# Performance work log

Hardware: AMD Instinct MI355X
Metric: run time of the kernel (lower is better)

## Reference

```python
import jax, jax.numpy as jnp
import numpy as np

D = 1024; NH = 16; HD = 64; FF = 4096; DEPTH = 4
P = 14; C = 3; GRID = 32; MERGE = 2; NIMG = 4
L = GRID * GRID; S = NIMG * L; ORIG = 24; EPS = 1e-6
SCALE = HD ** -0.5


def setup_inputs() -> dict:
    key = jax.random.key(0)
    ks = jax.random.split(key, 12)
    s = 0.02
    return {
        "pixel_values": jax.random.normal(ks[0], (S, C * P * P), jnp.float32),
        "grid_thw": jnp.tile(jnp.array([[1, GRID, GRID]], jnp.int32), (NIMG, 1)),
        "conv_w": jax.random.normal(ks[1], (D, C * P * P), jnp.float32) * s,
        "conv_b": jnp.zeros((D,), jnp.float32),
        "pos_embed": jax.random.normal(ks[2], (ORIG * ORIG, D), jnp.float32) * s,
        "ln1_g": jnp.ones((DEPTH, D), jnp.float32),
        "ln1_b": jnp.zeros((DEPTH, D), jnp.float32),
        "qkv_w": jax.random.normal(ks[3], (DEPTH, 3 * D, D), jnp.float32) * s,
        "qkv_b": jnp.zeros((DEPTH, 3 * D), jnp.float32),
        "proj_w": jax.random.normal(ks[4], (DEPTH, D, D), jnp.float32) * s,
        "proj_b": jnp.zeros((DEPTH, D), jnp.float32),
        "ln2_g": jnp.ones((DEPTH, D), jnp.float32),
        "ln2_b": jnp.zeros((DEPTH, D), jnp.float32),
        "fc1_w": jax.random.normal(ks[5], (DEPTH, FF, D), jnp.float32) * s,
        "fc1_b": jnp.zeros((DEPTH, FF), jnp.float32),
        "fc2_w": jax.random.normal(ks[6], (DEPTH, D, FF), jnp.float32) * s,
        "fc2_b": jnp.zeros((DEPTH, D), jnp.float32),
    }


def _pos_ids():
    # rot_pos_emb spatial-merge permutation for one t=1 image, tiled over images
    h = jnp.broadcast_to(jnp.arange(GRID)[:, None], (GRID, GRID))
    w = jnp.broadcast_to(jnp.arange(GRID)[None, :], (GRID, GRID))
    def perm(a):
        a = a.reshape(GRID // MERGE, MERGE, GRID // MERGE, MERGE)
        return a.transpose(0, 2, 1, 3).reshape(-1)
    hpos = jnp.tile(perm(h), NIMG)  # [S]
    wpos = jnp.tile(perm(w), NIMG)
    return hpos, wpos


def _bilinear_border(img, nx, ny):
    # img [H, W, D]; nx, ny in [-1, 1]; align_corners=False, padding_mode='border'
    Hh, Ww, _ = img.shape
    x = (nx + 1.0) * 0.5 * Ww - 0.5
    y = (ny + 1.0) * 0.5 * Hh - 0.5
    x0 = jnp.floor(x); y0 = jnp.floor(y)
    wx = (x - x0)[:, None]; wy = (y - y0)[:, None]
    x0i = jnp.clip(x0.astype(jnp.int32), 0, Ww - 1)
    x1i = jnp.clip(x0.astype(jnp.int32) + 1, 0, Ww - 1)
    y0i = jnp.clip(y0.astype(jnp.int32), 0, Hh - 1)
    y1i = jnp.clip(y0.astype(jnp.int32) + 1, 0, Hh - 1)
    v00 = img[y0i, x0i]; v01 = img[y0i, x1i]
    v10 = img[y1i, x0i]; v11 = img[y1i, x1i]
    return (v00 * (1 - wy) * (1 - wx) + v01 * (1 - wy) * wx
            + v10 * wy * (1 - wx) + v11 * wy * wx)


def _ln(x, g, b):
    m = jnp.mean(x, axis=-1, keepdims=True)
    v = jnp.mean(jnp.square(x - m), axis=-1, keepdims=True)
    return (x - m) * jax.lax.rsqrt(v + EPS) * g + b


def _forward(pixel_values, conv_w, conv_b, pos_embed, ln1_g, ln1_b, qkv_w, qkv_b,
             proj_w, proj_b, ln2_g, ln2_b, fc1_w, fc1_b, fc2_w, fc2_b):
    # patch embed: conv with kernel==stride==patch over one patch == linear
    x = pixel_values @ conv_w.T + conv_b  # [S, D]

    # interpolated 2D position embedding (grid_sample bilinear, border pad)
    hpos, wpos = _pos_ids()
    norm_w = (wpos.astype(jnp.float32) + 0.5) / GRID * 2.0 - 1.0
    norm_h = (hpos.astype(jnp.float32) + 0.5) / GRID * 2.0 - 1.0
    pe = _bilinear_border(pos_embed.reshape(ORIG, ORIG, D), norm_w, norm_h)
    x = x + pe

    for i in range(DEPTH):
        # attention (block-diagonal over equal-length images -> batched)
        r = x
        y = _ln(x, ln1_g[i], ln1_b[i])
        qkv = (y @ qkv_w[i].T + qkv_b[i]).reshape(NIMG, L, 3, NH, HD)
        q = qkv[:, :, 0].transpose(0, 2, 1, 3)  # [B, H, L, hd]
        k = qkv[:, :, 1].transpose(0, 2, 1, 3)
        v = qkv[:, :, 2].transpose(0, 2, 1, 3)
        scores = jnp.einsum('bhqd,bhkd->bhqk', q, k) * SCALE
        probs = jax.nn.softmax(scores, axis=-1)
        o = jnp.einsum('bhqk,bhkd->bhqd', probs, v)
        o = o.transpose(0, 2, 1, 3).reshape(S, D)
        x = r + o @ proj_w[i].T + proj_b[i]
        # MLP
        r = x
        y = _ln(x, ln2_g[i], ln2_b[i])
        h = jax.nn.gelu(y @ fc1_w[i].T + fc1_b[i], approximate=False)
        x = r + h @ fc2_w[i].T + fc2_b[i]
    return x


def reference(pixel_values, grid_thw, conv_w, conv_b, pos_embed, ln1_g, ln1_b,
              qkv_w, qkv_b, proj_w, proj_b, ln2_g, ln2_b, fc1_w, fc1_b, fc2_w, fc2_b):
    return _forward(pixel_values, conv_w, conv_b, pos_embed, ln1_g, ln1_b, qkv_w,
                    qkv_b, proj_w, proj_b, ln2_g, ln2_b, fc1_w, fc1_b, fc2_w, fc2_b)
```

## Files before the change

### kernel.cpp

```cpp
#include <hip/hip_runtime.h>
#include <math.h>

typedef __bf16 bf16x8 __attribute__((ext_vector_type(8)));
typedef float f32x4 __attribute__((ext_vector_type(4)));
typedef short s16x4 __attribute__((ext_vector_type(4)));
typedef short s16x8 __attribute__((ext_vector_type(8)));

static __device__ __forceinline__ short f2bs(float f) {
  return __builtin_bit_cast(short, (__bf16)f);
}

#define GLL16(gp, lp) __builtin_amdgcn_global_load_lds( \
    (const __attribute__((address_space(1))) void*)(gp), \
    (__attribute__((address_space(3))) void*)(lp), 16, 0, 0)

__global__ __launch_bounds__(256) void cvt_f32_bf16(const float* __restrict__ s,
                                                    short* __restrict__ d, int n) {
  int stride = gridDim.x * blockDim.x * 4;
  for (int j = (blockIdx.x * blockDim.x + threadIdx.x) * 4; j < n; j += stride) {
    float4 v = *(const float4*)(s + j);
    s16x4 o;
    o[0] = f2bs(v.x); o[1] = f2bs(v.y); o[2] = f2bs(v.z); o[3] = f2bs(v.w);
    *(s16x4*)(d + j) = o;
  }
}

__global__ __launch_bounds__(256) void cvt_pad(const float* __restrict__ s,
                                               short* __restrict__ d) {
  int r = blockIdx.x;
  for (int c = threadIdx.x; c < 608; c += blockDim.x)
    d[(size_t)r * 608 + c] = (c < 588) ? f2bs(s[(size_t)r * 588 + c]) : (short)0;
}

template <int N, int K, int EPI, int CM, int CN>
__global__ __launch_bounds__(256) void gemm_bt(const short* __restrict__ A,
                                               const short* __restrict__ B,
                                               const float* __restrict__ bias,
                                               const float* __restrict__ resid,
                                               void* __restrict__ out) {
  static_assert(K % 32 == 0, "K");
  constexpr int NT = K / 32;
  static_assert(NT >= 3, "pipeline depth");
  constexpr int NX = N / 128, NY = 32;
  constexpr int nwg = NX * NY;
  static_assert(nwg % 8 == 0 && (nwg / 8) % (CM * CN) == 0, "chunk");
  static_assert(NX % CN == 0 && NY % CM == 0, "cells");
  __shared__ short lA[3][128 * 32];
  __shared__ short lB[3][128 * 32];

  const int o = blockIdx.x;
  const int wid = (o & 7) * (nwg / 8) + (o >> 3);
  constexpr int cellsz = CM * CN;
  const int cell = wid / cellsz, within = wid % cellsz;
  constexpr int cellsx = NX / CN;
  const int bm0 = ((cell / cellsx) * CM + within / CN) * 128;
  const int bn0 = ((cell % cellsx) * CN + within % CN) * 128;

  const int t = threadIdx.x, w = t >> 6, lane = t & 63;
  const int wr = w >> 1, wc = w & 1;
  f32x4 acc[4][4] = {};

  const int srow = t >> 2;
  const int scol = ((t & 3) ^ ((srow >> 1) & 3)) * 8;
  const short* aP = A + (size_t)(bm0 + srow) * K + scol;
  const short* bP = B + (size_t)(bn0 + srow) * K + scol;
  const int sdst0 = (w * 16) * 32;
  const int sdst1 = (64 + w * 16) * 32;

  const int lr = lane & 15;
  const int qx = ((lane >> 4) ^ ((lr >> 1) & 3)) * 8;

  auto stage = [&](int buf, int ko) {
    GLL16(aP + ko, &lA[buf][sdst0]);
    GLL16(aP + ko + (size_t)64 * K, &lA[buf][sdst1]);
    GLL16(bP + ko, &lB[buf][sdst0]);
    GLL16(bP + ko + (size_t)64 * K, &lB[buf][sdst1]);
  };

  stage(0, 0);
  stage(1, 32);
  stage(2, 64);

  int buf = 0;
  for (int kt = 0; kt < NT; ++kt) {
    if (kt < NT - 2)       asm volatile("s_waitcnt vmcnt(8)" ::: "memory");
    else if (kt == NT - 2) asm volatile("s_waitcnt vmcnt(4)" ::: "memory");
    else                   asm volatile("s_waitcnt vmcnt(0)" ::: "memory");
    __builtin_amdgcn_s_barrier();
    asm volatile("" ::: "memory");
    __builtin_amdgcn_sched_barrier(0);

    bf16x8 af[4], bg[4];
#pragma unroll
    for (int mi = 0; mi < 4; ++mi)
      af[mi] = *(const bf16x8*)&lA[buf][(wr * 64 + mi * 16 + lr) * 32 + qx];
#pragma unroll
    for (int ni = 0; ni < 4; ++ni)
      bg[ni] = *(const bf16x8*)&lB[buf][(wc * 64 + ni * 16 + lr) * 32 + qx];

    asm volatile("s_waitcnt lgkmcnt(0)" ::: "memory");
    __builtin_amdgcn_sched_barrier(0);
    __builtin_amdgcn_s_barrier();
    asm volatile("" ::: "memory");
    __builtin_amdgcn_sched_barrier(0);

    if (kt + 3 < NT) stage(buf, (kt + 3) * 32);
    __builtin_amdgcn_sched_barrier(0);

#pragma unroll
    for (int mi = 0; mi < 4; ++mi)
#pragma unroll
      for (int ni = 0; ni < 4; ++ni)
        acc[mi][ni] = __builtin_amdgcn_mfma_f32_16x16x32_bf16(af[mi], bg[ni],
                                                              acc[mi][ni], 0, 0, 0);
    buf = (buf == 2) ? 0 : buf + 1;
  }

  const int lg4 = (lane >> 4) * 4;
#pragma unroll
  for (int mi = 0; mi < 4; ++mi) {
#pragma unroll
    for (int ni = 0; ni < 4; ++ni) {
      const int row = bm0 + wr * 64 + mi * 16 + lg4;
      const int col = bn0 + wc * 64 + ni * 16 + lr;
      const float bc = bias[col];
#pragma unroll
      for (int r = 0; r < 4; ++r) {
        float v = acc[mi][ni][r] + bc;
        size_t idx = (size_t)(row + r) * N + col;
        if constexpr (EPI == 1) v = 0.5f * v * (1.0f + erff(v * 0.70710678118f));
        if constexpr (EPI == 0 || EPI == 1) ((short*)out)[idx] = f2bs(v);
        else if constexpr (EPI == 2) ((float*)out)[idx] = v + resid[idx];
        else ((float*)out)[idx] = v;
      }
    }
  }
}

template <int N, int KC, int LDK, int EPI, int CM, int CN, int KSPLIT>
__global__ __launch_bounds__(512, 2) void gemm256(const short* __restrict__ A,
                                                  const short* __restrict__ B,
                                                  const float* __restrict__ bias,
                                                  void* __restrict__ out) {
  static_assert(KC % 64 == 0, "K");
  constexpr int NKT = KC / 64;
  static_assert(NKT >= 2, "ktiles");
  constexpr int NXT = N / 256, MYT = 16;
  constexpr int nwg = NXT * MYT * KSPLIT;
  constexpr int cellsz = CM * CN;
  static_assert(nwg % 8 == 0 && (nwg / 8) % cellsz == 0, "chunk");
  static_assert((NXT * MYT) % cellsz == 0, "cellspace");
  static_assert(NXT % CN == 0 && MYT % CM == 0, "cells");

  __shared__ short sA[2][2][8192];
  __shared__ short sB[2][2][8192];

  const int o = blockIdx.x;
  const int wid = (o & 7) * (nwg / 8) + (o >> 3);
  const int kc = wid / (NXT * MYT);
  const int rem = wid % (NXT * MYT);
  const int cell = rem / cellsz, within = rem % cellsz;
  constexpr int cellsx = NXT / CN;
  const int bm0 = ((cell / cellsx) * CM + within / CN) * 256;
  const int bn0 = ((cell % cellsx) * CN + within % CN) * 256;

  const int tid = threadIdx.x, wv = tid >> 6, lane = tid & 63;
  const int wrow = wv >> 2, wcol = wv & 3;
  const int lr = lane & 15, lg = lane >> 4;

  const int sr0 = tid >> 2;
  const int sc0 = ((tid & 3) ^ ((sr0 >> 1) & 3)) * 8;
  const short* aS0 = A + (size_t)(bm0 + sr0) * LDK + kc * KC + sc0;
  const short* bS0 = B + (size_t)(bn0 + sr0) * LDK + kc * KC + sc0;
  const int ld0 = wv * 512, ld1 = 4096 + wv * 512;

  auto stageA = [&](int d, int h, int kt) {
    const int off = kt * 64 + h * 32;
    GLL16(aS0 + off, &sA[d][h][ld0]);
    GLL16(aS0 + off + (size_t)128 * LDK, &sA[d][h][ld1]);
  };
  auto stageB = [&](int d, int h, int kt) {
    const int off = kt * 64 + h * 32;
    GLL16(bS0 + off, &sB[d][h][ld0]);
    GLL16(bS0 + off + (size_t)128 * LDK, &sB[d][h][ld1]);
  };

  const int chR = (lg ^ ((lr >> 1) & 3)) * 8;
  const int rA0 = wrow * 128 + lr;
  const int rB0 = wcol * 64 + lr;

  f32x4 acc[8][4] = {};
  bf16x8 aF[4][2], bF[4][2];

  stageA(0, 0, 0); stageA(0, 1, 0);
  stageB(0, 0, 0); stageB(0, 1, 0);
  asm volatile("s_waitcnt vmcnt(0)" ::: "memory");
  __builtin_amdgcn_s_barrier();

#define RD_A(mh)                                                              \
  _Pragma("unroll")                                                           \
  for (int f = 0; f < 4; ++f) {                                               \
    aF[f][0] = *(const bf16x8*)&sA[r][0][(rA0 + (mh)*64 + f * 16) * 32 + chR];\
    aF[f][1] = *(const bf16x8*)&sA[r][1][(rA0 + (mh)*64 + f * 16) * 32 + chR];\
  }
#define RD_B2(n0)                                                             \
  _Pragma("unroll")                                                           \
  for (int n = 0; n < 2; ++n) {                                               \
    bF[(n0)+n][0] = *(const bf16x8*)&sB[r][0][(rB0 + ((n0)+n) * 16) * 32 + chR];\
    bF[(n0)+n][1] = *(const bf16x8*)&sB[r][1][(rB0 + ((n0)+n) * 16) * 32 + chR];\
  }
#define MM(ab, n0)                                                            \
  __builtin_amdgcn_s_setprio(1);                                              \
  _Pragma("unroll")                                                           \
  for (int ks = 0; ks < 2; ++ks)                                              \
    _Pragma("unroll")                                                         \
    for (int f = 0; f < 4; ++f)                                               \
      _Pragma("unroll")                                                       \
      for (int n = 0; n < 2; ++n)                                             \
        acc[(ab)+f][(n0)+n] = __builtin_amdgcn_mfma_f32_16x16x32_bf16(        \
            aF[f][ks], bF[(n0)+n][ks], acc[(ab)+f][(n0)+n], 0, 0, 0);         \
  __builtin_amdgcn_s_setprio(0);
#define BAR __builtin_amdgcn_s_barrier();
#define LGW asm volatile("s_waitcnt lgkmcnt(0)");

  for (int t = 0; t < NKT; ++t) {
    const int r = t & 1, sd = r ^ 1;
    const bool more = (t + 1 < NKT);
    RD_A(0); RD_B2(0);
    if (more) { stageA(sd, 0, t + 1); stageA(sd, 1, t + 1); }
    BAR; LGW; MM(0, 0); BAR;
    RD_B2(2);
    if (more) { stageB(sd, 0, t + 1); stageB(sd, 1, t + 1); }
    BAR; LGW; MM(0, 2); BAR;
    RD_A(1);
    BAR; LGW; MM(4, 2); BAR;
    MM(4, 0);
    asm volatile("s_waitcnt vmcnt(0)" ::: "memory");
    BAR;
  }
#undef RD_A
#undef RD_B2
#undef MM
#undef BAR
#undef LGW

  const int lg4 = lg * 4;
#pragma unroll
  for (int mh = 0; mh < 2; ++mh) {
#pragma unroll
    for (int f = 0; f < 4; ++f) {
#pragma unroll
      for (int n = 0; n < 4; ++n) {
        const int row = bm0 + wrow * 128 + mh * 64 + f * 16 + lg4;
        const int col = bn0 + wcol * 64 + n * 16 + lr;
        float bc = 0.f;
        if constexpr (EPI != 5) bc = bias[col];
#pragma unroll
        for (int r = 0; r < 4; ++r) {
          float v = acc[mh * 4 + f][n][r] + bc;
          if constexpr (EPI == 1) {
            const float u = v * (0.7978845608f + 0.0356774081f * v * v);
            v = v / (1.0f + __expf(-2.0f * u));
          }
          if constexpr (EPI == 5)
            ((float*)out)[((size_t)kc << 22) + (size_t)(row + r) * N + col] = v;
          else
            ((short*)out)[(size_t)(row + r) * N + col] = f2bs(v);
        }
      }
    }
  }
}

__global__ __launch_bounds__(256) void fc2_reduce(const float* __restrict__ part,
                                                  const float* __restrict__ bias,
                                                  const float* __restrict__ resid,
                                                  float* __restrict__ dest) {
  const size_t i4 = ((size_t)blockIdx.x * 256 + threadIdx.x) * 4;
  const float4 a0 = *(const float4*)(part + i4);
  const float4 a1 = *(const float4*)(part + (1ull << 22) + i4);
  const float4 a2 = *(const float4*)(part + (2ull << 22) + i4);
  const float4 a3 = *(const float4*)(part + (3ull << 22) + i4);
  const float4 rv = *(const float4*)(resid + i4);
  const float4 bv = *(const float4*)(bias + (i4 & 1023));
  float4 o;
  o.x = a0.x + a1.x + a2.x + a3.x + rv.x + bv.x;
  o.y = a0.y + a1.y + a2.y + a3.y + rv.y + bv.y;
  o.z = a0.z + a1.z + a2.z + a3.z + rv.z + bv.z;
  o.w = a0.w + a1.w + a2.w + a3.w + rv.w + bv.w;
  *(float4*)(dest + i4) = o;
}

__global__ __launch_bounds__(256) void ln_fwd(const float* __restrict__ x,
                                              const float* __restrict__ g,
                                              const float* __restrict__ b,
                                              short* __restrict__ y) {
  const int row = blockIdx.x, t = threadIdx.x, w = t >> 6, lane = t & 63;
  const float4 v = ((const float4*)(x + (size_t)row * 1024))[t];
  float s = v.x + v.y + v.z + v.w;
  float ss = v.x * v.x + v.y * v.y + v.z * v.z + v.w * v.w;
#pragma unroll
  for (int m = 1; m < 64; m <<= 1) { s += __shfl_xor(s, m); ss += __shfl_xor(ss, m); }
  __shared__ float rs[4], rss[4];
  if (lane == 0) { rs[w] = s; rss[w] = ss; }
  __syncthreads();
  s = rs[0] + rs[1] + rs[2] + rs[3];
  ss = rss[0] + rss[1] + rss[2] + rss[3];
  const float mean = s * (1.f / 1024.f);
  const float var = ss * (1.f / 1024.f) - mean * mean;
  const float rstd = rsqrtf(var + 1e-6f);
  const float4 gv = ((const float4*)g)[t];
  const float4 bv = ((const float4*)b)[t];
  s16x4 o;
  o[0] = f2bs((v.x - mean) * rstd * gv.x + bv.x);
  o[1] = f2bs((v.y - mean) * rstd * gv.y + bv.y);
  o[2] = f2bs((v.z - mean) * rstd * gv.z + bv.z);
  o[3] = f2bs((v.w - mean) * rstd * gv.w + bv.w);
  *(s16x4*)(y + (size_t)row * 1024 + t * 4) = o;
}

__global__ __launch_bounds__(256) void pos_add(float* __restrict__ x,
                                               const float* __restrict__ pe) {
  const int sidx = blockIdx.x;
  const int f = sidx & 1023;
  const int wq = 2 * ((f >> 2) & 15) + (f & 1);
  const int hq = 2 * (f >> 6) + ((f >> 1) & 1);
  const float gx = (wq + 0.5f) * 0.75f - 0.5f;
  const float gy = (hq + 0.5f) * 0.75f - 0.5f;
  const float fx = floorf(gx), fy = floorf(gy);
  const float wx = gx - fx, wy = gy - fy;
  int x0 = (int)fx, y0 = (int)fy;
  const int x0i = x0 < 0 ? 0 : (x0 > 23 ? 23 : x0);
  const int x1i = (x0 + 1) < 0 ? 0 : ((x0 + 1) > 23 ? 23 : x0 + 1);
  const int y0i = y0 < 0 ? 0 : (y0 > 23 ? 23 : y0);
  const int y1i = (y0 + 1) < 0 ? 0 : ((y0 + 1) > 23 ? 23 : y0 + 1);
  const float w00 = (1 - wy) * (1 - wx), w01 = (1 - wy) * wx;
  const float w10 = wy * (1 - wx), w11 = wy * wx;
  const int c = threadIdx.x * 4;
  const float4 p00 = *(const float4*)(pe + (size_t)(y0i * 24 + x0i) * 1024 + c);
  const float4 p01 = *(const float4*)(pe + (size_t)(y0i * 24 + x1i) * 1024 + c);
  const float4 p10 = *(const float4*)(pe + (size_t)(y1i * 24 + x0i) * 1024 + c);
  const float4 p11 = *(const float4*)(pe + (size_t)(y1i * 24 + x1i) * 1024 + c);
  float* xp = x + (size_t)sidx * 1024 + c;
  float4 xv = *(float4*)xp;
  xv.x += w00 * p00.x + w01 * p01.x + w10 * p10.x + w11 * p11.x;
  xv.y += w00 * p00.y + w01 * p01.y + w10 * p10.y + w11 * p11.y;
  xv.z += w00 * p00.z + w01 * p01.z + w10 * p10.z + w11 * p11.z;
  xv.w += w00 * p00.w + w01 * p01.w + w10 * p10.w + w11 * p11.w;
  *(float4*)xp = xv;
}

__global__ __launch_bounds__(256) void attn_fwd(const short* __restrict__ qkv,
                                                short* __restrict__ outp) {
  __shared__ short lK[2][64 * 64];
  __shared__ short Vt[2][64 * 72];
  const int t = threadIdx.x, w = t >> 6, lane = t & 63;
  const int b = blockIdx.y >> 4, h = blockIdx.y & 15;
  const int sbase = b * 1024;
  const int q0 = blockIdx.x * 64 + w * 16;
  const int lr = lane & 15, lg = lane >> 4;

  const short* qrow = qkv + (size_t)(sbase + q0 + lr) * 3072 + h * 64;
  const bf16x8 qf0 = *(const bf16x8*)(qrow + lg * 8);
  const bf16x8 qf1 = *(const bf16x8*)(qrow + 32 + lg * 8);

  const int krofs = t >> 3;
  const int kcol = ((t & 7) ^ (krofs & 7)) * 8;
  const short* ksrc = qkv + (size_t)(sbase + krofs) * 3072 + 1024 + h * 64 + kcol;
  const int vkv = t >> 2, vdp = t & 3;
  const short* vsrc = qkv + (size_t)(sbase + vkv) * 3072 + 2048 + h * 64 + vdp * 16;
  const int vph = vkv ^ (vdp << 4);

  f32x4 o[4] = {};
  float mrun = -1e30f, lsum = 0.f;

  s16x8 v0 = *(const s16x8*)vsrc;
  s16x8 v1 = *(const s16x8*)(vsrc + 8);
  GLL16(ksrc, &lK[0][(w * 8) * 64]);
  GLL16(ksrc + (size_t)32 * 3072, &lK[0][(32 + w * 8) * 64]);
#pragma unroll
  for (int j = 0; j < 8; ++j) Vt[0][(vdp * 16 + j) * 72 + vph] = v0[j];
#pragma unroll
  for (int j = 0; j < 8; ++j) Vt[0][(vdp * 16 + 8 + j) * 72 + vph] = v1[j];
  asm volatile("s_waitcnt vmcnt(0) lgkmcnt(0)" ::: "memory");
  __builtin_amdgcn_s_barrier();

  int buf = 0;
  for (int kb = 0; kb < 16; ++kb) {
    if (kb < 15) {
      const short* vs = vsrc + (size_t)(kb + 1) * 64 * 3072;
      v0 = *(const s16x8*)vs;
      v1 = *(const s16x8*)(vs + 8);
      const short* ks = ksrc + (size_t)(kb + 1) * 64 * 3072;
      GLL16(ks, &lK[buf ^ 1][(w * 8) * 64]);
      GLL16(ks + (size_t)32 * 3072, &lK[buf ^ 1][(32 + w * 8) * 64]);
    }

    f32x4 s[4];
    __builtin_amdgcn_s_setprio(1);
#pragma unroll
    for (int sub = 0; sub < 4; ++sub) {
      const int krow = (sub * 16 + lr) * 64;
      const bf16x8 kf0 = *(const bf16x8*)&lK[buf][krow + (lg ^ (lr & 7)) * 8];
      const bf16x8 kf1 = *(const bf16x8*)&lK[buf][krow + ((lg + 4) ^ (lr & 7)) * 8];
      f32x4 a = {};
      a = __builtin_amdgcn_mfma_f32_16x16x32_bf16(kf0, qf0, a, 0, 0, 0);
      a = __builtin_amdgcn_mfma_f32_16x16x32_bf16(kf1, qf1, a, 0, 0, 0);
      s[sub] = a;
    }
    __builtin_amdgcn_s_setprio(0);

    constexpr float SC = 0.125f * 1.44269504089f;
    float sl[16];
#pragma unroll
    for (int sub = 0; sub < 4; ++sub)
#pragma unroll
      for (int r = 0; r < 4; ++r) sl[sub * 4 + r] = s[sub][r] * SC;
    float tm = sl[0];
#pragma unroll
    for (int i = 1; i < 16; ++i) tm = fmaxf(tm, sl[i]);
    tm = fmaxf(tm, __shfl_xor(tm, 16));
    tm = fmaxf(tm, __shfl_xor(tm, 32));
    if (!__all(tm <= mrun + 12.0f)) {
      const float newm = fmaxf(mrun, tm);
      const float sc = exp2f(mrun - newm);
      lsum *= sc;
#pragma unroll
      for (int f = 0; f < 4; ++f) {
        o[f][0] *= sc; o[f][1] *= sc; o[f][2] *= sc; o[f][3] *= sc;
      }
      mrun = newm;
    }
    s16x4 pb[4];
    float psum = 0.f;
#pragma unroll
    for (int sub = 0; sub < 4; ++sub)
#pragma unroll
      for (int r = 0; r < 4; ++r) {
        const float p = exp2f(sl[sub * 4 + r] - mrun);
        psum += p;
        pb[sub][r] = f2bs(p);
      }
    psum += __shfl_xor(psum, 16);
    psum += __shfl_xor(psum, 32);
    lsum += psum;

    __builtin_amdgcn_s_setprio(1);
#pragma unroll
    for (int f = 0; f < 4; ++f) {
      const int vrow = (f * 16 + lr) * 72;
#pragma unroll
      for (int sub = 0; sub < 4; ++sub) {
        const s16x4 va = *(const s16x4*)&Vt[buf][vrow + ((sub ^ f) << 4) + lg * 4];
        o[f] = __builtin_amdgcn_mfma_f32_16x16x16bf16_1k(va, pb[sub], o[f], 0, 0, 0);
      }
    }
    __builtin_amdgcn_s_setprio(0);

    if (kb < 15) {
#pragma unroll
      for (int j = 0; j < 8; ++j) Vt[buf ^ 1][(vdp * 16 + j) * 72 + vph] = v0[j];
#pragma unroll
      for (int j = 0; j < 8; ++j) Vt[buf ^ 1][(vdp * 16 + 8 + j) * 72 + vph] = v1[j];
      asm volatile("s_waitcnt vmcnt(0) lgkmcnt(0)" ::: "memory");
      __builtin_amdgcn_s_barrier();
      buf ^= 1;
    }
  }

  const float inv = 1.0f / lsum;
  short* orow = outp + (size_t)(sbase + q0 + lr) * 1024 + h * 64;
#pragma unroll
  for (int f = 0; f < 4; ++f) {
    s16x4 ov;
    ov[0] = f2bs(o[f][0] * inv); ov[1] = f2bs(o[f][1] * inv);
    ov[2] = f2bs(o[f][2] * inv); ov[3] = f2bs(o[f][3] * inv);
    *(s16x4*)(orow + f * 16 + lg * 4) = ov;
  }
}

extern "C" void kernel_launch(void* const* d_in, const int* in_sizes, int n_in,
                              void* d_out, int out_size, void* d_ws, size_t ws_size,
                              hipStream_t stream) {
  const float* pixel  = (const float*)d_in[0];
  const float* conv_w = (const float*)d_in[2];
  const float* conv_b = (const float*)d_in[3];
  const float* pos_e  = (const float*)d_in[4];
  const float* ln1_g  = (const float*)d_in[5];
  const float* ln1_b  = (const float*)d_in[6];
  const float* qkv_w  = (const float*)d_in[7];
  const float* qkv_b  = (const float*)d_in[8];
  const float* proj_w = (const float*)d_in[9];
  const float* proj_b = (const float*)d_in[10];
  const float* ln2_g  = (const float*)d_in[11];
  const float* ln2_b  = (const float*)d_in[12];
  const float* fc1_w  = (const float*)d_in[13];
  const float* fc1_b  = (const float*)d_in[14];
  const float* fc2_w  = (const float*)d_in[15];
  const float* fc2_b  = (const float*)d_in[16];

  char* ws = (char*)d_ws;
  short* wQKV  = (short*)(ws + 0);
  short* wPROJ = (short*)(ws + 25165824);
  short* wFC1  = (short*)(ws + 33554432);
  short* wFC2  = (short*)(ws + 67108864);
  float* X     = (float*)(ws + 100663296);
  short* Y     = (short*)(ws + 117440512);
  short* QKVB  = (short*)(ws + 125829120);
  short* ATTNO = (short*)(ws + 150994944);
  short* H     = QKVB;
  short* WPIX  = QKVB;
  short* WCONV = (short*)(ws + 125829120 + 4980736);
  float* PART  = (float*)(ws + 159383552);
  const bool wsbig = ws_size >= (size_t)159383552 + 67108864;

  cvt_f32_bf16<<<2048, 256, 0, stream>>>(qkv_w, wQKV, 4 * 3072 * 1024);
  cvt_f32_bf16<<<1024, 256, 0, stream>>>(proj_w, wPROJ, 4 * 1024 * 1024);
  cvt_f32_bf16<<<2048, 256, 0, stream>>>(fc1_w, wFC1, 4 * 4096 * 1024);
  cvt_f32_bf16<<<2048, 256, 0, stream>>>(fc2_w, wFC2, 4 * 1024 * 4096);
  cvt_pad<<<4096, 256, 0, stream>>>(pixel, WPIX);
  cvt_pad<<<1024, 256, 0, stream>>>(conv_w, WCONV);

  gemm_bt<1024, 608, 3, 4, 8><<<256, 256, 0, stream>>>(WPIX, WCONV, conv_b, nullptr, X);
  pos_add<<<4096, 256, 0, stream>>>(X, pos_e);

  for (int i = 0; i < 4; ++i) {
    ln_fwd<<<4096, 256, 0, stream>>>(X, ln1_g + i * 1024, ln1_b + i * 1024, Y);
    gemm256<3072, 1024, 1024, 0, 8, 3, 1><<<192, 512, 0, stream>>>(
        Y, wQKV + (size_t)i * 3072 * 1024, qkv_b + i * 3072, QKVB);
    attn_fwd<<<dim3(16, 64), 256, 0, stream>>>(QKVB, ATTNO);
    gemm_bt<1024, 1024, 2, 4, 8><<<256, 256, 0, stream>>>(
        ATTNO, wPROJ + (size_t)i * 1024 * 1024, proj_b + i * 1024, X, X);
    ln_fwd<<<4096, 256, 0, stream>>>(X, ln2_g + i * 1024, ln2_b + i * 1024, Y);
    gemm256<4096, 1024, 1024, 1, 8, 4, 1><<<256, 512, 0, stream>>>(
        Y, wFC1 + (size_t)i * 4096 * 1024, fc1_b + i * 4096, H);
    float* dest = (i < 3) ? X : (float*)d_out;
    if (wsbig) {
      gemm256<1024, 1024, 4096, 5, 8, 4, 4><<<256, 512, 0, stream>>>(
          H, wFC2 + (size_t)i * 1024 * 4096, nullptr, PART);
      fc2_reduce<<<4096, 256, 0, stream>>>(PART, fc2_b + i * 1024, X, dest);
    } else {
      gemm_bt<1024, 4096, 2, 4, 8><<<256, 256, 0, stream>>>(
          H, wFC2 + (size_t)i * 1024 * 4096, fc2_b + i * 1024, X, dest);
    }
  }
}
```

Baseline: 973.6 us.

## Split-K proj GEMM with new 128-tile kernel and fuse residual reduce into LayerNorm

Adds a 128x128-tile split-K GEMM kernel for the attention output projection, which writes four fp32 partials. A new reduce_ln kernel sums those partials with bias and residual, writes X, and computes the next LayerNorm in the same pass. The same fusion is applied after the fc2 split-K reduce, so the standalone ln_fwd launches and their extra read of X go away. The cost is more partial-buffer traffic for proj (4x fp32 writes) in exchange for better occupancy with 1024 workgroups.

Result: no change. 990.0 us (+1.7%).

```diff
diff --git a/kernel.cpp b/kernel.cpp
--- a/kernel.cpp
+++ b/kernel.cpp
@@ -132,6 +132,120 @@
         if constexpr (EPI == 0 || EPI == 1) ((short*)out)[idx] = f2bs(v);
         else if constexpr (EPI == 2) ((float*)out)[idx] = v + resid[idx];
         else ((float*)out)[idx] = v;
+      }
+    }
+  }
+}
+
+template <int N, int KC, int LDK, int EPI, int CM, int CN, int KSPLIT>
+__global__ __launch_bounds__(256, 2) void gemm128(const short* __restrict__ A,
+                                                  const short* __restrict__ B,
+                                                  const float* __restrict__ bias,
+                                                  void* __restrict__ out) {
+  static_assert(KC % 64 == 0, "K");
+  constexpr int NKT = KC / 64;
+  static_assert(NKT >= 4 && (NKT % 2) == 0, "ktiles");
+  constexpr int NX = N / 128, NY = 32;
+  constexpr int nwg = NX * NY * KSPLIT;
+  constexpr int cellsz = CM * CN;
+  static_assert(nwg % 8 == 0 && (nwg / 8) % cellsz == 0, "chunk");
+  static_assert((NX * NY) % cellsz == 0, "cellspace");
+  static_assert(NX % CN == 0 && NY % CM == 0, "cells");
+
+  __shared__ short sA[2][128 * 64];
+  __shared__ short sB[2][128 * 64];
+
+  const int o = blockIdx.x;
+  const int wid = (o & 7) * (nwg / 8) + (o >> 3);
+  const int kc = wid / (NX * NY);
+  const int rem = wid % (NX * NY);
+  const int cell = rem / cellsz, within = rem % cellsz;
+  constexpr int cellsx = NX / CN;
+  const int bm0 = ((cell / cellsx) * CM + within / CN) * 128;
+  const int bn0 = ((cell % cellsx) * CN + within % CN) * 128;
+
+  const int t = threadIdx.x, w = t >> 6, lane = t & 63;
+  const int wr = w >> 1, wc = w & 1;
+  const int lr = lane & 15, lg = lane >> 4;
+
+  const int srow = t >> 3;
+  const int sch = (t & 7) ^ (srow & 7);
+  const short* aS = A + (size_t)(bm0 + srow) * LDK + kc * KC + sch * 8;
+  const short* bS = B + (size_t)(bn0 + srow) * LDK + kc * KC + sch * 8;
+  const int ldst = w * 512;
+
+  auto stage = [&](int d, int kt) {
+    const size_t ko = (size_t)kt * 64;
+#pragma unroll
+    for (int q = 0; q < 4; ++q)
+      GLL16(aS + (size_t)q * 32 * LDK + ko, &sA[d][q * 2048 + ldst]);
+#pragma unroll
+    for (int q = 0; q < 4; ++q)
+      GLL16(bS + (size_t)q * 32 * LDK + ko, &sB[d][q * 2048 + ldst]);
+  };
+
+  f32x4 acc[4][4] = {};
+
+  stage(0, 0);
+  stage(1, 1);
+
+#define TILE(tt, dd)                                                          \
+  {                                                                           \
+    if ((tt) + 1 < NKT) asm volatile("s_waitcnt vmcnt(8)" ::: "memory");      \
+    else                asm volatile("s_waitcnt vmcnt(0)" ::: "memory");      \
+    __builtin_amdgcn_s_barrier();                                             \
+    bf16x8 af[2][4], bf[2][4];                                                \
+    _Pragma("unroll")                                                         \
+    for (int ks = 0; ks < 2; ++ks) {                                          \
+      _Pragma("unroll")                                                       \
+      for (int mi = 0; mi < 4; ++mi)                                          \
+        af[ks][mi] = *(const bf16x8*)&sA[dd][(wr * 64 + mi * 16 + lr) * 64 +  \
+                                             (((ks << 2) + lg) ^ (lr & 7)) * 8]; \
+      _Pragma("unroll")                                                       \
+      for (int ni = 0; ni < 4; ++ni)                                          \
+        bf[ks][ni] = *(const bf16x8*)&sB[dd][(wc * 64 + ni * 16 + lr) * 64 +  \
+                                             (((ks << 2) + lg) ^ (lr & 7)) * 8]; \
+    }                                                                         \
+    __builtin_amdgcn_s_setprio(1);                                            \
+    _Pragma("unroll")                                                         \
+    for (int ks = 0; ks < 2; ++ks)                                            \
+      _Pragma("unroll")                                                       \
+      for (int mi = 0; mi < 4; ++mi)                                          \
+        _Pragma("unroll")                                                     \
+        for (int ni = 0; ni < 4; ++ni)                                        \
+          acc[mi][ni] = __builtin_amdgcn_mfma_f32_16x16x32_bf16(              \
+              af[ks][mi], bf[ks][ni], acc[mi][ni], 0, 0, 0);                  \
+    __builtin_amdgcn_s_setprio(0);                                            \
+    __builtin_amdgcn_s_barrier();                                             \
+    if ((tt) + 2 < NKT) stage(dd, (tt) + 2);                                  \
+  }
+
+  for (int kt = 0; kt < NKT; kt += 2) {
+    TILE(kt, 0);
+    TILE(kt + 1, 1);
+  }
+#undef TILE
+
+  const int lg4 = lg * 4;
+#pragma unroll
+  for (int mi = 0; mi < 4; ++mi) {
+#pragma unroll
+    for (int ni = 0; ni < 4; ++ni) {
+      const int row = bm0 + wr * 64 + mi * 16 + lg4;
+      const int col = bn0 + wc * 64 + ni * 16 + lr;
+      float bc = 0.f;
+      if constexpr (EPI != 5) bc = bias[col];
+#pragma unroll
+      for (int r = 0; r < 4; ++r) {
+        float v = acc[mi][ni][r] + bc;
+        if constexpr (EPI == 1) {
+          const float u = v * (0.7978845608f + 0.0356774081f * v * v);
+          v = v / (1.0f + __expf(-2.0f * u));
+        }
+        if constexpr (EPI == 5)
+          ((float*)out)[((size_t)kc << 22) + (size_t)(row + r) * N + col] = v;
+        else
+          ((short*)out)[(size_t)(row + r) * N + col] = f2bs(v);
       }
     }
   }
@@ -289,6 +403,50 @@
   o.z = a0.z + a1.z + a2.z + a3.z + rv.z + bv.z;
   o.w = a0.w + a1.w + a2.w + a3.w + rv.w + bv.w;
   *(float4*)(dest + i4) = o;
+}
+
+__global__ __launch_bounds__(256) void reduce_ln(const float* __restrict__ part,
+                                                 const float* __restrict__ bias,
+                                                 const float* __restrict__ resid,
+                                                 const float* __restrict__ g,
+                                                 const float* __restrict__ b,
+                                                 float* __restrict__ X,
+                                                 short* __restrict__ Y) {
+  const int row = blockIdx.x, t = threadIdx.x, w = t >> 6, lane = t & 63;
+  const size_t i4 = (size_t)row * 1024 + t * 4;
+  const float4 a0 = *(const float4*)(part + i4);
+  const float4 a1 = *(const float4*)(part + (1ull << 22) + i4);
+  const float4 a2 = *(const float4*)(part + (2ull << 22) + i4);
+  const float4 a3 = *(const float4*)(part + (3ull << 22) + i4);
+  const float4 rv = *(const float4*)(resid + i4);
+  const float4 bv = *(const float4*)(bias + t * 4);
+  float4 v;
+  v.x = a0.x + a1.x + a2.x + a3.x + rv.x + bv.x;
+  v.y = a0.y + a1.y + a2.y + a3.y + rv.y + bv.y;
+  v.z = a0.z + a1.z + a2.z + a3.z + rv.z + bv.z;
+  v.w = a0.w + a1.w + a2.w + a3.w + rv.w + bv.w;
+  *(float4*)(X + i4) = v;
+
+  float s = v.x + v.y + v.z + v.w;
+  float ss = v.x * v.x + v.y * v.y + v.z * v.z + v.w * v.w;
+#pragma unroll
+  for (int m = 1; m < 64; m <<= 1) { s += __shfl_xor(s, m); ss += __shfl_xor(ss, m); }
+  __shared__ float rs[4], rss[4];
+  if (lane == 0) { rs[w] = s; rss[w] = ss; }
+  __syncthreads();
+  s = rs[0] + rs[1] + rs[2] + rs[3];
+  ss = rss[0] + rss[1] + rss[2] + rss[3];
+  const float mean = s * (1.f / 1024.f);
+  const float var = ss * (1.f / 1024.f) - mean * mean;
+  const float rstd = rsqrtf(var + 1e-6f);
+  const float4 gv = ((const float4*)g)[t];
+  const float4 bb = ((const float4*)b)[t];
+  s16x4 o;
+  o[0] = f2bs((v.x - mean) * rstd * gv.x + bb.x);
+  o[1] = f2bs((v.y - mean) * rstd * gv.y + bb.y);
+  o[2] = f2bs((v.z - mean) * rstd * gv.z + bb.z);
+  o[3] = f2bs((v.w - mean) * rstd * gv.w + bb.w);
+  *(s16x4*)(Y + i4) = o;
 }
 
 __global__ __launch_bounds__(256) void ln_fwd(const float* __restrict__ x,
@@ -523,25 +681,45 @@
 
   gemm_bt<1024, 608, 3, 4, 8><<<256, 256, 0, stream>>>(WPIX, WCONV, conv_b, nullptr, X);
   pos_add<<<4096, 256, 0, stream>>>(X, pos_e);
+  ln_fwd<<<4096, 256, 0, stream>>>(X, ln1_g, ln1_b, Y);
 
   for (int i = 0; i < 4; ++i) {
-    ln_fwd<<<4096, 256, 0, stream>>>(X, ln1_g + i * 1024, ln1_b + i * 1024, Y);
     gemm256<3072, 1024, 1024, 0, 8, 3, 1><<<192, 512, 0, stream>>>(
         Y, wQKV + (size_t)i * 3072 * 1024, qkv_b + i * 3072, QKVB);
     attn_fwd<<<dim3(16, 64), 256, 0, stream>>>(QKVB, ATTNO);
-    gemm_bt<1024, 1024, 2, 4, 8><<<256, 256, 0, stream>>>(
-        ATTNO, wPROJ + (size_t)i * 1024 * 1024, proj_b + i * 1024, X, X);
-    ln_fwd<<<4096, 256, 0, stream>>>(X, ln2_g + i * 1024, ln2_b + i * 1024, Y);
+
+    if (wsbig) {
+      gemm128<1024, 256, 1024, 5, 8, 4, 4><<<1024, 256, 0, stream>>>(
+          ATTNO, wPROJ + (size_t)i * 1024 * 1024, nullptr, PART);
+      reduce_ln<<<4096, 256, 0, stream>>>(PART, proj_b + i * 1024, X,
+                                          ln2_g + i * 1024, ln2_b + i * 1024, X, Y);
+    } else {
+      gemm_bt<1024, 1024, 2, 4, 8><<<256, 256, 0, stream>>>(
+          ATTNO, wPROJ + (size_t)i * 1024 * 1024, proj_b + i * 1024, X, X);
+      ln_fwd<<<4096, 256, 0, stream>>>(X, ln2_g + i * 1024, ln2_b + i * 1024, Y);
+    }
+
     gemm256<4096, 1024, 1024, 1, 8, 4, 1><<<256, 512, 0, stream>>>(
         Y, wFC1 + (size_t)i * 4096 * 1024, fc1_b + i * 4096, H);
-    float* dest = (i < 3) ? X : (float*)d_out;
+
     if (wsbig) {
       gemm256<1024, 1024, 4096, 5, 8, 4, 4><<<256, 512, 0, stream>>>(
           H, wFC2 + (size_t)i * 1024 * 4096, nullptr, PART);
-      fc2_reduce<<<4096, 256, 0, stream>>>(PART, fc2_b + i * 1024, X, dest);
+      if (i < 3) {
+        reduce_ln<<<4096, 256, 0, stream>>>(PART, fc2_b + i * 1024, X,
+                                            ln1_g + (i + 1) * 1024,
+                                            ln1_b + (i + 1) * 1024, X, Y);
+      } else {
+        fc2_reduce<<<4096, 256, 0, stream>>>(PART, fc2_b + i * 1024, X,
+                                             (float*)d_out);
+      }
     } else {
+      float* dest = (i < 3) ? X : (float*)d_out;
       gemm_bt<1024, 4096, 2, 4, 8><<<256, 256, 0, stream>>>(
           H, wFC2 + (size_t)i * 1024 * 4096, fc2_b + i * 1024, X, dest);
-    }
-  }
-}
+      if (i < 3)
+        ln_fwd<<<4096, 256, 0, stream>>>(X, ln1_g + (i + 1) * 1024,
+                                         ln1_b + (i + 1) * 1024, Y);
+    }
+  }
+}
```
